# Performance work log

Measured on AMD Instinct MI355X. Metric: run time of the kernel, lower is better.

## Reference

```python
import jax, jax.numpy as jnp
import numpy as np
from jax import lax

NPOINT = 256   # num_proposal
RADIUS = 0.3
NSAMPLE = 16
B, K, C = 32, 1024, 256
OUT_CH = 2 + 3 + 1 * 2 + 18 * 4 + 18  # 97


def _fps(xyz, npoint):
    """Furthest point sampling. xyz (B,N,3) -> indices (B,npoint) int32."""
    b, n, _ = xyz.shape

    def step(carry, _):
        dist, far = carry
        centroid = jnp.take_along_axis(xyz, far[:, None, None], axis=1)  # (B,1,3)
        d = jnp.sum((xyz - centroid) ** 2, -1)
        dist = jnp.minimum(dist, d)
        nxt = jnp.argmax(dist, -1).astype(jnp.int32)
        return (dist, nxt), far

    init = (jnp.full((b, n), 1e10, xyz.dtype), jnp.zeros((b,), jnp.int32))
    _, inds = lax.scan(step, init, None, length=npoint)
    return jnp.transpose(inds)  # (B,npoint)


def _ball_query(new_xyz, xyz, radius, nsample):
    """pointnet2-style ball query: first nsample in-radius neighbors (by point
    order), slots past the count filled with the first found index."""
    n = xyz.shape[1]
    # squared dists (B,P,N) without materializing (B,P,N,3)
    d2 = (jnp.sum(new_xyz ** 2, -1)[:, :, None]
          + jnp.sum(xyz ** 2, -1)[:, None, :]
          - 2.0 * jnp.einsum('bpc,bnc->bpn', new_xyz, xyz))
    key = jnp.where(d2 < radius * radius, jnp.arange(n)[None, None, :], n)
    order = jnp.argsort(key, axis=-1)[:, :, :nsample]
    skey = jnp.take_along_axis(key, order, axis=-1)
    first = order[:, :, :1]
    return jnp.where(skey < n, order, first)  # (B,P,ns)


def _gather_nbrs(pts, idx):
    """pts (B,N,Cd), idx (B,P,ns) -> (B,P,ns,Cd)."""
    b, p, s = idx.shape
    flat = idx.reshape(b, p * s)
    g = jnp.take_along_axis(pts, flat[:, :, None], axis=1)
    return g.reshape(b, p, s, pts.shape[-1])


def setup_inputs() -> dict:
    key = jax.random.key(0)
    ks = jax.random.split(key, 24)
    f32 = jnp.float32

    def w(k, o, c):
        return (jax.random.normal(k, (o, c), f32) / np.float32(np.sqrt(c)))

    def affine(k, o):
        k1, k2 = jax.random.split(k)
        s = 1.0 + 0.1 * jax.random.normal(k1, (o,), f32)
        t = 0.1 * jax.random.normal(k2, (o,), f32)
        return s, t

    d = {}
    d['xyz'] = jax.random.normal(ks[0], (B, K, 3), f32)
    d['features'] = jax.random.normal(ks[1], (B, C, K), f32)
    # SA shared-MLP (conv2d 1x1 + folded eval-mode BN): [C+3 -> 128 -> 128 -> 128]
    d['sa_w0'] = w(ks[2], 128, C + 3); d['sa_s0'], d['sa_t0'] = affine(ks[3], 128)
    d['sa_w1'] = w(ks[4], 128, 128);   d['sa_s1'], d['sa_t1'] = affine(ks[5], 128)
    d['sa_w2'] = w(ks[6], 128, 128);   d['sa_s2'], d['sa_t2'] = affine(ks[7], 128)
    # head conv1d stack: conv1/bn1, conv2/bn2 (BN folded), conv3 with bias
    d['w1'] = w(ks[8], 128, 128); d['s1'], d['t1'] = affine(ks[9], 128)
    d['w2'] = w(ks[10], 128, 128); d['s2'], d['t2'] = affine(ks[11], 128)
    d['w3'] = w(ks[12], OUT_CH, 128)
    d['b3'] = 0.1 * jax.random.normal(ks[13], (OUT_CH,), f32)
    return d


def reference(xyz, features, sa_w0, sa_s0, sa_t0, sa_w1, sa_s1, sa_t1,
              sa_w2, sa_s2, sa_t2, w1, s1, t1, w2, s2, t2, w3, b3):
    # --- PointnetSAModuleVotes (vote_fps branch): FPS + ball query + group ---
    inds = _fps(xyz, NPOINT)                                    # (B,P)
    new_xyz = jnp.take_along_axis(xyz, inds[:, :, None], axis=1)  # (B,P,3)
    idx = _ball_query(new_xyz, xyz, RADIUS, NSAMPLE)            # (B,P,ns)
    # use_xyz=True, normalize_xyz=True
    gx = (_gather_nbrs(xyz, idx) - new_xyz[:, :, None, :]) / RADIUS   # (B,P,ns,3)
    gf = _gather_nbrs(jnp.transpose(features, (0, 2, 1)), idx)        # (B,P,ns,C)
    x = jnp.concatenate([gx, gf], axis=-1)                            # (B,P,ns,C+3)
    # shared MLP (1x1 conv + BN + ReLU), then max-pool over neighbors
    for W, s, t in ((sa_w0, sa_s0, sa_t0), (sa_w1, sa_s1, sa_t1), (sa_w2, sa_s2, sa_t2)):
        x = jax.nn.relu(jnp.einsum('oc,bpnc->bpno', W, x) * s + t)
    f = jnp.transpose(jnp.max(x, axis=2), (0, 2, 1))  # (B,128,P)
    # --- proposal head: conv1d/BN/ReLU x2 + conv1d ---
    h = jax.nn.relu(jnp.einsum('oc,bcp->bop', w1, f) * s1[:, None] + t1[:, None])
    h = jax.nn.relu(jnp.einsum('oc,bcp->bop', w2, h) * s2[:, None] + t2[:, None])
    net = jnp.einsum('oc,bcp->bop', w3, h) + b3[:, None]  # (B,97,P)
    return net
```

## Files before the change

### kernel.cpp

```cpp
#include <hip/hip_runtime.h>

#define NB 32
#define NPTS 1024
#define NP 256
#define NS 16
#define NC 256
#define NH 128
#define NOUT 97
#define RP 16
#define NT (NB * NP)

__global__ __launch_bounds__(256) void prep_kernel(
    const float* __restrict__ sa_w0, const float* __restrict__ sa_w1,
    const float* __restrict__ sa_w2, const float* __restrict__ fc_w1,
    const float* __restrict__ fc_w2, const float* __restrict__ fc_w3,
    float* __restrict__ w0l, float* __restrict__ w0x,
    float* __restrict__ wl1, float* __restrict__ wl2,
    float* __restrict__ fl1, float* __restrict__ fl2,
    float* __restrict__ fl3)
{
  int t = blockIdx.x * 256 + threadIdx.x;
  if (t >= 256 * 128) return;
  int c = t >> 7, o = t & 127;
  w0l[(c * 32 + (o & 31)) * 4 + (o >> 5)] = sa_w0[o * 259 + 3 + c];
  if (c < 3) w0x[c * 128 + o] = sa_w0[o * 259 + c];
  if (c < 128) {
    int qi = (c * 64 + (o & 63)) * 2 + (o >> 6);
    wl1[qi] = sa_w1[o * 128 + c];
    wl2[qi] = sa_w2[o * 128 + c];
    fl1[qi] = fc_w1[o * 128 + c];
    fl2[qi] = fc_w2[o * 128 + c];
    fl3[qi] = (o < NOUT) ? fc_w3[o * 128 + c] : 0.0f;
  }
}

template <int CTRL>
__device__ __forceinline__ float dpp_fmax(float v) {
  float o = __int_as_float(
      __builtin_amdgcn_mov_dpp(__float_as_int(v), CTRL, 0xF, 0xF, true));
  return fmaxf(v, o);
}
template <int CTRL>
__device__ __forceinline__ unsigned dpp_umax(unsigned v) {
  unsigned o = (unsigned)__builtin_amdgcn_mov_dpp((int)v, CTRL, 0xF, 0xF, true);
  return v > o ? v : o;
}

__global__ __launch_bounds__(64) void fused_fps_gfeat_kernel(
    const float* __restrict__ xyz, int* __restrict__ inds,
    const float* __restrict__ features, const float* __restrict__ w0l,
    float* __restrict__ G)
{
  __shared__ __align__(16) float smem[NC * RP];
  const int lane = threadIdx.x;

  if (blockIdx.x < NB) {
    const int b = blockIdx.x;
    const float* xb = xyz + b * NPTS * 3;
    float* s_x = smem;
    float* s_y = smem + NPTS;
    float* s_z = smem + 2 * NPTS;
    float px[16], py[16], pz[16], dist[16];
    const float4* src = reinterpret_cast<const float4*>(xb + lane * 48);
#pragma unroll
    for (int q = 0; q < 4; ++q) {
      float4 v0 = src[3 * q], v1 = src[3 * q + 1], v2 = src[3 * q + 2];
      const float xv[4] = {v0.x, v0.w, v1.z, v2.y};
      const float yv[4] = {v0.y, v1.x, v1.w, v2.z};
      const float zv[4] = {v0.z, v1.y, v2.x, v2.w};
#pragma unroll
      for (int t = 0; t < 4; ++t) {
        int j = 4 * q + t;
        px[j] = xv[t]; py[j] = yv[t]; pz[j] = zv[t];
        s_x[lane * 16 + j] = xv[t];
        s_y[lane * 16 + j] = yv[t];
        s_z[lane * 16 + j] = zv[t];
      }
    }
#pragma unroll
    for (int j = 0; j < 16; ++j) dist[j] = 1e10f;
    int far = 0;
    for (int i = 0; i < NP; ++i) {
      if (lane == 0) inds[b * NP + i] = far;
      float cx = s_x[far], cy = s_y[far], cz = s_z[far];
      float bv = -1.0f; int bi = 0;
#pragma unroll
      for (int j = 0; j < 16; ++j) {
#pragma clang fp contract(off)
        float dx = px[j] - cx;
        float dy = py[j] - cy;
        float dz = pz[j] - cz;
        float d = (dx * dx + dy * dy) + dz * dz;
        float nd = fminf(dist[j], d);
        dist[j] = nd;
        if (nd > bv) { bv = nd; bi = lane * 16 + j; }
      }
      float r = bv;
      r = dpp_fmax<0x111>(r);
      r = dpp_fmax<0x112>(r);
      r = dpp_fmax<0x114>(r);
      r = dpp_fmax<0x118>(r);
      r = dpp_fmax<0x142>(r);
      r = dpp_fmax<0x143>(r);
      float gmax = __int_as_float(__builtin_amdgcn_readlane(__float_as_int(r), 63));
      unsigned cand = (bv == gmax) ? ~(unsigned)bi : 0u;
      cand = dpp_umax<0x111>(cand);
      cand = dpp_umax<0x112>(cand);
      cand = dpp_umax<0x114>(cand);
      cand = dpp_umax<0x118>(cand);
      cand = dpp_umax<0x142>(cand);
      cand = dpp_umax<0x143>(cand);
      unsigned cmax = (unsigned)__builtin_amdgcn_readlane((int)cand, 63);
      far = (int)(~cmax);
    }
    return;
  }

  const int blk = blockIdx.x - NB;
  const int b  = blk >> 6;
  const int n0 = (blk & 63) * 16;
  const int og = lane & 31;
  const int jg = lane >> 5;
  const int joff = jg * 8;
  const float* fb = features + b * NC * NPTS;
#pragma unroll
  for (int r = 0; r < 4; ++r) {
    int c = r * 64 + lane;
    const float4* s4 = reinterpret_cast<const float4*>(fb + c * NPTS + n0);
    float4 v0 = s4[0], v1 = s4[1], v2 = s4[2], v3 = s4[3];
    float* row = smem + c * RP;
    reinterpret_cast<float4*>(row)[0] = v0;
    reinterpret_cast<float4*>(row)[1] = v1;
    reinterpret_cast<float4*>(row)[2] = v2;
    reinterpret_cast<float4*>(row)[3] = v3;
  }
  float acc[4][8];
#pragma unroll
  for (int k = 0; k < 4; ++k)
#pragma unroll
    for (int nn = 0; nn < 8; ++nn) acc[k][nn] = 0.0f;
#pragma unroll 2
  for (int c = 0; c < NC; ++c) {
    const float4 wq = *reinterpret_cast<const float4*>(w0l + (c * 32 + og) * 4);
    const float* row = smem + c * RP + joff;
    const float4 xa = reinterpret_cast<const float4*>(row)[0];
    const float4 xb4 = reinterpret_cast<const float4*>(row)[1];
    const float wk[4] = {wq.x, wq.y, wq.z, wq.w};
    const float xr[8] = {xa.x, xa.y, xa.z, xa.w, xb4.x, xb4.y, xb4.z, xb4.w};
#pragma unroll
    for (int k = 0; k < 4; ++k)
#pragma unroll
      for (int nn = 0; nn < 8; ++nn)
        acc[k][nn] = fmaf(wk[k], xr[nn], acc[k][nn]);
  }
#pragma unroll
  for (int k = 0; k < 4; ++k) {
    int o = og + 32 * k;
    float* gp = G + ((size_t)(b * NPTS + n0 + joff)) * NH + o;
#pragma unroll
    for (int nn = 0; nn < 8; ++nn) gp[nn * NH] = acc[k][nn];
  }
}

__global__ __launch_bounds__(256) void ball_kernel(
    const float* __restrict__ xyz, const int* __restrict__ inds,
    int* __restrict__ nbr, float* __restrict__ gx, int* __restrict__ totals)
{
  const int wid  = blockIdx.x * 4 + (threadIdx.x >> 6);
  const int lane = threadIdx.x & 63;
  const int b = wid >> 8;
  const float* xb = xyz + b * NPTS * 3;
  const int ci = inds[wid];
  const float cx = xb[ci * 3 + 0], cy = xb[ci * 3 + 1], cz = xb[ci * 3 + 2];
  float nq;
  {
#pragma clang fp contract(off)
    nq = (cx * cx + cy * cy) + cz * cz;
  }
  const float R2 = 0.09f;
  unsigned mask = 0;
  int cntj = 0, firstn = NPTS;
  for (int j = 0; j < 16; ++j) {
#pragma clang fp contract(off)
    int n = lane * 16 + j;
    float x = xb[n * 3 + 0], y = xb[n * 3 + 1], z = xb[n * 3 + 2];
    float nx = (x * x + y * y) + z * z;
    float dt = (cx * x + cy * y) + cz * z;
    float d2 = (nq + nx) - 2.0f * dt;
    if (d2 < R2) { mask |= 1u << j; ++cntj; if (firstn == NPTS) firstn = n; }
  }
  int inc = cntj;
  for (int off = 1; off < 64; off <<= 1) {
    int v = __shfl_up(inc, off);
    if (lane >= off) inc += v;
  }
  int rank  = inc - cntj;
  int total = __shfl(inc, 63);
  for (int j = 0; j < 16; ++j) {
    if (mask & (1u << j)) {
      if (rank < NS) {
        int n = lane * 16 + j;
        nbr[wid * NS + rank] = n;
        float x = xb[n * 3 + 0], y = xb[n * 3 + 1], z = xb[n * 3 + 2];
        gx[wid * 48 + rank * 3 + 0] = (x - cx) / 0.3f;
        gx[wid * 48 + rank * 3 + 1] = (y - cy) / 0.3f;
        gx[wid * 48 + rank * 3 + 2] = (z - cz) / 0.3f;
      }
      ++rank;
    }
  }
  int fmin = firstn;
  for (int off2 = 32; off2 > 0; off2 >>= 1) {
    int ov = __shfl_xor(fmin, off2);
    fmin = min(fmin, ov);
  }
  if (lane < NS && lane >= total) {
    nbr[wid * NS + lane] = fmin;
    float x = xb[fmin * 3 + 0], y = xb[fmin * 3 + 1], z = xb[fmin * 3 + 2];
    gx[wid * 48 + lane * 3 + 0] = (x - cx) / 0.3f;
    gx[wid * 48 + lane * 3 + 1] = (y - cy) / 0.3f;
    gx[wid * 48 + lane * 3 + 2] = (z - cz) / 0.3f;
  }
  if (lane == 0) totals[wid] = total;
}

__global__ __launch_bounds__(1024) void scan_kernel(
    const int* __restrict__ totals, int* __restrict__ bucket, int* __restrict__ cnt)
{
  __shared__ unsigned long long ssum[16];
  const int t = threadIdx.x;
  int cls[8];
  unsigned long long local = 0;
#pragma unroll
  for (int k = 0; k < 8; ++k) {
    int tot = totals[t * 8 + k];
    int jc = (tot <= 4) ? 0 : ((tot <= 8) ? 1 : 2);
    cls[k] = jc;
    local += 1ull << (jc * 21);
  }
  unsigned long long inc = local;
  for (int off = 1; off < 64; off <<= 1) {
    unsigned long long v = __shfl_up(inc, off);
    if ((t & 63) >= off) inc += v;
  }
  if ((t & 63) == 63) ssum[t >> 6] = inc;
  __syncthreads();
  if (t == 0) {
    unsigned long long run = 0;
    for (int i = 0; i < 16; ++i) { unsigned long long v = ssum[i]; ssum[i] = run; run += v; }
    cnt[0] = (int)(run & 0x1FFFFFull);
    cnt[1] = (int)((run >> 21) & 0x1FFFFFull);
    cnt[2] = (int)((run >> 42) & 0x1FFFFFull);
  }
  __syncthreads();
  unsigned long long excl = (inc - local) + ssum[t >> 6];
  int p0 = (int)(excl & 0x1FFFFFull);
  int p1 = (int)((excl >> 21) & 0x1FFFFFull);
  int p2 = (int)((excl >> 42) & 0x1FFFFFull);
#pragma unroll
  for (int k = 0; k < 8; ++k) {
    int id = t * 8 + k;
    if (cls[k] == 0)      { bucket[p0] = id; ++p0; }
    else if (cls[k] == 1) { bucket[NT + p1] = id; ++p1; }
    else                  { bucket[2 * NT + p2] = id; ++p2; }
  }
}

__device__ __forceinline__ void mlp16(
    float* __restrict__ xs, const int lane,
    const float* __restrict__ G, const int* __restrict__ idxw,
    const float* __restrict__ gxw,
    const float* __restrict__ w0x, const float* __restrict__ s0v, const float* __restrict__ t0v,
    const float* __restrict__ wl1, const float* __restrict__ s1v, const float* __restrict__ t1v,
    const float* __restrict__ wl2,
    float acc0[16], float acc1[16])
{
  {
    const float wa0 = w0x[lane],      wb0 = w0x[128 + lane],      wc0 = w0x[256 + lane];
    const float wa1 = w0x[64 + lane], wb1 = w0x[192 + lane],      wc1 = w0x[320 + lane];
    const float ss0 = s0v[lane], tt0 = t0v[lane];
    const float ss1 = s0v[64 + lane], tt1 = t0v[64 + lane];
    float r0[16], r1[16];
#pragma unroll
    for (int j = 0; j < 16; ++j) {
      int gj = idxw[j];
      float gxv = gxw[j * 3 + 0], gyv = gxw[j * 3 + 1], gzv = gxw[j * 3 + 2];
      const float* gp = G + (size_t)gj * NH;
      float g0 = gp[lane], g1 = gp[lane + 64];
      float y0 = fmaf(wa0, gxv, fmaf(wb0, gyv, fmaf(wc0, gzv, g0)));
      float y1 = fmaf(wa1, gxv, fmaf(wb1, gyv, fmaf(wc1, gzv, g1)));
      r0[j] = fmaxf(fmaf(y0, ss0, tt0), 0.0f);
      r1[j] = fmaxf(fmaf(y1, ss1, tt1), 0.0f);
    }
#pragma unroll
    for (int q = 0; q < 4; ++q) {
      *reinterpret_cast<float4*>(xs + lane * RP + q * 4) =
          make_float4(r0[4 * q], r0[4 * q + 1], r0[4 * q + 2], r0[4 * q + 3]);
      *reinterpret_cast<float4*>(xs + (lane + 64) * RP + q * 4) =
          make_float4(r1[4 * q], r1[4 * q + 1], r1[4 * q + 2], r1[4 * q + 3]);
    }
  }

#pragma unroll
  for (int j = 0; j < 16; ++j) { acc0[j] = 0.0f; acc1[j] = 0.0f; }
#pragma unroll 2
  for (int c = 0; c < NH; ++c) {
    const float2 wv = *reinterpret_cast<const float2*>(wl1 + (c * 64 + lane) * 2);
#pragma unroll
    for (int q = 0; q < 4; ++q) {
      const float4 xq = *reinterpret_cast<const float4*>(xs + c * RP + q * 4);
      acc0[4 * q + 0] = fmaf(wv.x, xq.x, acc0[4 * q + 0]);
      acc1[4 * q + 0] = fmaf(wv.y, xq.x, acc1[4 * q + 0]);
      acc0[4 * q + 1] = fmaf(wv.x, xq.y, acc0[4 * q + 1]);
      acc1[4 * q + 1] = fmaf(wv.y, xq.y, acc1[4 * q + 1]);
      acc0[4 * q + 2] = fmaf(wv.x, xq.z, acc0[4 * q + 2]);
      acc1[4 * q + 2] = fmaf(wv.y, xq.z, acc1[4 * q + 2]);
      acc0[4 * q + 3] = fmaf(wv.x, xq.w, acc0[4 * q + 3]);
      acc1[4 * q + 3] = fmaf(wv.y, xq.w, acc1[4 * q + 3]);
    }
  }
  {
    const float ssa = s1v[lane], tta = t1v[lane];
    const float ssb = s1v[64 + lane], ttb = t1v[64 + lane];
#pragma unroll
    for (int q = 0; q < 4; ++q) {
      float4 ra, rb;
      ra.x = fmaxf(fmaf(acc0[4 * q + 0], ssa, tta), 0.0f);
      ra.y = fmaxf(fmaf(acc0[4 * q + 1], ssa, tta), 0.0f);
      ra.z = fmaxf(fmaf(acc0[4 * q + 2], ssa, tta), 0.0f);
      ra.w = fmaxf(fmaf(acc0[4 * q + 3], ssa, tta), 0.0f);
      rb.x = fmaxf(fmaf(acc1[4 * q + 0], ssb, ttb), 0.0f);
      rb.y = fmaxf(fmaf(acc1[4 * q + 1], ssb, ttb), 0.0f);
      rb.z = fmaxf(fmaf(acc1[4 * q + 2], ssb, ttb), 0.0f);
      rb.w = fmaxf(fmaf(acc1[4 * q + 3], ssb, ttb), 0.0f);
      *reinterpret_cast<float4*>(xs + lane * RP + q * 4) = ra;
      *reinterpret_cast<float4*>(xs + (lane + 64) * RP + q * 4) = rb;
    }
  }

#pragma unroll
  for (int j = 0; j < 16; ++j) { acc0[j] = 0.0f; acc1[j] = 0.0f; }
#pragma unroll 2
  for (int c = 0; c < NH; ++c) {
    const float2 wv = *reinterpret_cast<const float2*>(wl2 + (c * 64 + lane) * 2);
#pragma unroll
    for (int q = 0; q < 4; ++q) {
      const float4 xq = *reinterpret_cast<const float4*>(xs + c * RP + q * 4);
      acc0[4 * q + 0] = fmaf(wv.x, xq.x, acc0[4 * q + 0]);
      acc1[4 * q + 0] = fmaf(wv.y, xq.x, acc1[4 * q + 0]);
      acc0[4 * q + 1] = fmaf(wv.x, xq.y, acc0[4 * q + 1]);
      acc1[4 * q + 1] = fmaf(wv.y, xq.y, acc1[4 * q + 1]);
      acc0[4 * q + 2] = fmaf(wv.x, xq.z, acc0[4 * q + 2]);
      acc1[4 * q + 2] = fmaf(wv.y, xq.z, acc1[4 * q + 2]);
      acc0[4 * q + 3] = fmaf(wv.x, xq.w, acc0[4 * q + 3]);
      acc1[4 * q + 3] = fmaf(wv.y, xq.w, acc1[4 * q + 3]);
    }
  }
}

template <int TPW>
__device__ __forceinline__ void fc_epilogue(
    float* __restrict__ xs, const int lane, const int tiles[4],
    float acc0[16], float acc1[16],
    const float* __restrict__ s2v, const float* __restrict__ t2v,
    const float* __restrict__ fl1, const float* __restrict__ fs1, const float* __restrict__ ft1,
    const float* __restrict__ fl2, const float* __restrict__ fs2, const float* __restrict__ ft2,
    const float* __restrict__ fl3, const float* __restrict__ b3, float* __restrict__ out)
{
  constexpr int SPT = 16 / TPW;
  {
    const float ssa = s2v[lane], tta = t2v[lane];
    const float ssb = s2v[64 + lane], ttb = t2v[64 + lane];
#pragma unroll
    for (int k = 0; k < TPW; ++k) {
      float fo0 = 0.0f, fo1 = 0.0f;
#pragma unroll
      for (int r = 0; r < SPT; ++r) {
        fo0 = fmaxf(fo0, fmaxf(fmaf(acc0[k * SPT + r], ssa, tta), 0.0f));
        fo1 = fmaxf(fo1, fmaxf(fmaf(acc1[k * SPT + r], ssb, ttb), 0.0f));
      }
      xs[k * 128 + lane] = fo0;
      xs[k * 128 + 64 + lane] = fo1;
    }
  }
  constexpr int HB = TPW * 128;

  float h0[TPW], h1[TPW];

#pragma unroll
  for (int k = 0; k < TPW; ++k) { h0[k] = 0.0f; h1[k] = 0.0f; }
#pragma unroll 4
  for (int c4 = 0; c4 < 32; ++c4) {
    float4 fq[TPW];
#pragma unroll
    for (int k = 0; k < TPW; ++k)
      fq[k] = *reinterpret_cast<const float4*>(xs + k * 128 + c4 * 4);
#pragma unroll
    for (int cc = 0; cc < 4; ++cc) {
      const float2 wv = *reinterpret_cast<const float2*>(fl1 + ((c4 * 4 + cc) * 64 + lane) * 2);
#pragma unroll
      for (int k = 0; k < TPW; ++k) {
        float fv = (cc == 0) ? fq[k].x : (cc == 1) ? fq[k].y : (cc == 2) ? fq[k].z : fq[k].w;
        h0[k] = fmaf(wv.x, fv, h0[k]);
        h1[k] = fmaf(wv.y, fv, h1[k]);
      }
    }
  }
#pragma unroll
  for (int k = 0; k < TPW; ++k) {
    xs[HB + k * 128 + lane]      = fmaxf(fmaf(h0[k], fs1[lane],      ft1[lane]),      0.0f);
    xs[HB + k * 128 + 64 + lane] = fmaxf(fmaf(h1[k], fs1[lane + 64], ft1[lane + 64]), 0.0f);
  }

#pragma unroll
  for (int k = 0; k < TPW; ++k) { h0[k] = 0.0f; h1[k] = 0.0f; }
#pragma unroll 4
  for (int c4 = 0; c4 < 32; ++c4) {
    float4 fq[TPW];
#pragma unroll
    for (int k = 0; k < TPW; ++k)
      fq[k] = *reinterpret_cast<const float4*>(xs + HB + k * 128 + c4 * 4);
#pragma unroll
    for (int cc = 0; cc < 4; ++cc) {
      const float2 wv = *reinterpret_cast<const float2*>(fl2 + ((c4 * 4 + cc) * 64 + lane) * 2);
#pragma unroll
      for (int k = 0; k < TPW; ++k) {
        float fv = (cc == 0) ? fq[k].x : (cc == 1) ? fq[k].y : (cc == 2) ? fq[k].z : fq[k].w;
        h0[k] = fmaf(wv.x, fv, h0[k]);
        h1[k] = fmaf(wv.y, fv, h1[k]);
      }
    }
  }
#pragma unroll
  for (int k = 0; k < TPW; ++k) {
    xs[k * 128 + lane]      = fmaxf(fmaf(h0[k], fs2[lane],      ft2[lane]),      0.0f);
    xs[k * 128 + 64 + lane] = fmaxf(fmaf(h1[k], fs2[lane + 64], ft2[lane + 64]), 0.0f);
  }

#pragma unroll
  for (int k = 0; k < TPW; ++k) { h0[k] = 0.0f; h1[k] = 0.0f; }
#pragma unroll 4
  for (int c4 = 0; c4 < 32; ++c4) {
    float4 fq[TPW];
#pragma unroll
    for (int k = 0; k < TPW; ++k)
      fq[k] = *reinterpret_cast<const float4*>(xs + k * 128 + c4 * 4);
#pragma unroll
    for (int cc = 0; cc < 4; ++cc) {
      const float2 wv = *reinterpret_cast<const float2*>(fl3 + ((c4 * 4 + cc) * 64 + lane) * 2);
#pragma unroll
      for (int k = 0; k < TPW; ++k) {
        float fv = (cc == 0) ? fq[k].x : (cc == 1) ? fq[k].y : (cc == 2) ? fq[k].z : fq[k].w;
        h0[k] = fmaf(wv.x, fv, h0[k]);
        h1[k] = fmaf(wv.y, fv, h1[k]);
      }
    }
  }
#pragma unroll
  for (int k = 0; k < TPW; ++k) {
    int tk = tiles[k];
    int b = tk >> 8, p = tk & 255;
    out[(b * NOUT + lane) * NP + p] = h0[k] + b3[lane];
    if (lane < NOUT - 64)
      out[(b * NOUT + lane + 64) * NP + p] = h1[k] + b3[lane + 64];
  }
}

__global__ __launch_bounds__(512) void main_kernel(
    const int* __restrict__ nbr, const float* __restrict__ gx,
    const int* __restrict__ bucket, const int* __restrict__ cnt,
    const float* __restrict__ G,
    const float* __restrict__ w0x, const float* __restrict__ s0v, const float* __restrict__ t0v,
    const float* __restrict__ wl1, const float* __restrict__ s1v, const float* __restrict__ t1v,
    const float* __restrict__ wl2, const float* __restrict__ s2v, const float* __restrict__ t2v,
    const float* __restrict__ fl1, const float* __restrict__ fs1, const float* __restrict__ ft1,
    const float* __restrict__ fl2, const float* __restrict__ fs2, const float* __restrict__ ft2,
    const float* __restrict__ fl3, const float* __restrict__ b3, float* __restrict__ out)
{
  __shared__ __align__(16) float xt[8][NH * RP];
  __shared__ float gxs[8][NS][3];
  __shared__ int   idxs[8][NS];

  const int w    = threadIdx.x >> 6;
  const int lane = threadIdx.x & 63;
  const int g    = blockIdx.x * 8 + w;

  const int c0 = cnt[0], c1 = cnt[1], c2 = cnt[2];
  const int npack4 = (c0 + 3) >> 2;
  const int npack8 = (c1 + 1) >> 1;
  if (g >= npack4 + npack8 + c2) return;

  int tiles[4];
  int tpw;
  if (g < npack4) {
    tpw = 4;
    tiles[0] = bucket[min(4 * g + 0, c0 - 1)];
    tiles[1] = bucket[min(4 * g + 1, c0 - 1)];
    tiles[2] = bucket[min(4 * g + 2, c0 - 1)];
    tiles[3] = bucket[min(4 * g + 3, c0 - 1)];
  } else if (g < npack4 + npack8) {
    tpw = 2;
    int base = g - npack4;
    tiles[0] = bucket[NT + min(2 * base + 0, c1 - 1)];
    tiles[1] = bucket[NT + min(2 * base + 1, c1 - 1)];
    tiles[2] = tiles[0]; tiles[3] = tiles[1];
  } else {
    tpw = 1;
    tiles[0] = bucket[2 * NT + (g - npack4 - npack8)];
    tiles[1] = tiles[2] = tiles[3] = tiles[0];
  }

  float* xs = &xt[w][0];

  if (lane < 16) {
    int tk, r;
    if (tpw == 4)      { tk = (lane < 4) ? tiles[0] : (lane < 8) ? tiles[1]
                              : (lane < 12) ? tiles[2] : tiles[3];  r = lane & 3; }
    else if (tpw == 2) { tk = (lane < 8) ? tiles[0] : tiles[1];     r = lane & 7; }
    else               { tk = tiles[0];                              r = lane; }
    int bk = tk >> 8;
    idxs[w][lane] = bk * NPTS + nbr[tk * NS + r];
    gxs[w][lane][0] = gx[tk * 48 + r * 3 + 0];
    gxs[w][lane][1] = gx[tk * 48 + r * 3 + 1];
    gxs[w][lane][2] = gx[tk * 48 + r * 3 + 2];
  }

  float acc0[16], acc1[16];
  mlp16(xs, lane, G, idxs[w], &gxs[w][0][0],
        w0x, s0v, t0v, wl1, s1v, t1v, wl2, acc0, acc1);

  if (tpw == 4) {
    fc_epilogue<4>(xs, lane, tiles, acc0, acc1, s2v, t2v,
                   fl1, fs1, ft1, fl2, fs2, ft2, fl3, b3, out);
  } else if (tpw == 2) {
    fc_epilogue<2>(xs, lane, tiles, acc0, acc1, s2v, t2v,
                   fl1, fs1, ft1, fl2, fs2, ft2, fl3, b3, out);
  } else {
    fc_epilogue<1>(xs, lane, tiles, acc0, acc1, s2v, t2v,
                   fl1, fs1, ft1, fl2, fs2, ft2, fl3, b3, out);
  }
}

extern "C" void kernel_launch(void* const* d_in, const int* in_sizes, int n_in,
                              void* d_out, int out_size, void* d_ws, size_t ws_size,
                              hipStream_t stream) {
  const float* xyz      = (const float*)d_in[0];
  const float* features = (const float*)d_in[1];
  const float* sa_w0 = (const float*)d_in[2];
  const float* sa_s0 = (const float*)d_in[3];
  const float* sa_t0 = (const float*)d_in[4];
  const float* sa_w1 = (const float*)d_in[5];
  const float* sa_s1 = (const float*)d_in[6];
  const float* sa_t1 = (const float*)d_in[7];
  const float* sa_w2 = (const float*)d_in[8];
  const float* sa_s2 = (const float*)d_in[9];
  const float* sa_t2 = (const float*)d_in[10];
  const float* fc_w1 = (const float*)d_in[11];
  const float* fc_s1 = (const float*)d_in[12];
  const float* fc_t1 = (const float*)d_in[13];
  const float* fc_w2 = (const float*)d_in[14];
  const float* fc_s2 = (const float*)d_in[15];
  const float* fc_t2 = (const float*)d_in[16];
  const float* fc_w3 = (const float*)d_in[17];
  const float* fc_b3 = (const float*)d_in[18];
  float* out = (float*)d_out;

  char* ws = (char*)d_ws;
  int* inds = (int*)ws;            ws += (size_t)NT * sizeof(int);
  float* w0l  = (float*)ws;        ws += (size_t)256 * 128 * sizeof(float);
  float* w0x  = (float*)ws;        ws += (size_t)3 * 128 * sizeof(float);
  float* wl1  = (float*)ws;        ws += (size_t)128 * 128 * sizeof(float);
  float* wl2  = (float*)ws;        ws += (size_t)128 * 128 * sizeof(float);
  float* fl1  = (float*)ws;        ws += (size_t)128 * 128 * sizeof(float);
  float* fl2  = (float*)ws;        ws += (size_t)128 * 128 * sizeof(float);
  float* fl3  = (float*)ws;        ws += (size_t)128 * 128 * sizeof(float);
  float* G    = (float*)ws;        ws += (size_t)NB * NPTS * NH * sizeof(float);
  int*   nbr  = (int*)ws;          ws += (size_t)NT * NS * sizeof(int);
  float* gx   = (float*)ws;        ws += (size_t)NT * 48 * sizeof(float);
  int* totals = (int*)ws;          ws += (size_t)NT * sizeof(int);
  int* bucket = (int*)ws;          ws += (size_t)3 * NT * sizeof(int);
  int* cnt    = (int*)ws;          ws += 16 * sizeof(int);

  prep_kernel<<<128, 256, 0, stream>>>(sa_w0, sa_w1, sa_w2, fc_w1, fc_w2, fc_w3,
                                       w0l, w0x, wl1, wl2, fl1, fl2, fl3);
  fused_fps_gfeat_kernel<<<NB + NB * (NPTS / 16), 64, 0, stream>>>(
      xyz, inds, features, w0l, G);
  ball_kernel<<<NT / 4, 256, 0, stream>>>(xyz, inds, nbr, gx, totals);
  scan_kernel<<<1, 1024, 0, stream>>>(totals, bucket, cnt);
  main_kernel<<<NT / 8, 512, 0, stream>>>(
      nbr, gx, bucket, cnt, G,
      w0x, sa_s0, sa_t0,
      wl1, sa_s1, sa_t1,
      wl2, sa_s2, sa_t2,
      fl1, fc_s1, fc_t1,
      fl2, fc_s2, fc_t2,
      fl3, fc_b3, out);
}
```

Baseline: 251.9 us.

## Split FPS into own kernel, fuse feature GEMM with ball query, tree argmax

FPS moves into a standalone kernel. The first-layer feature projection (G) is no longer fused with FPS; it now shares a launch with the ball query, which runs as one 64-thread block per centroid. The per-lane argmax inside FPS becomes a pairwise tree reduction instead of a sequential compare chain, which shortens the dependency chain on the serial FPS critical path. The cost is that the G projection can no longer overlap FPS: it now waits until FPS finishes, which may lengthen the critical path.

```diff
diff --git a/kernel.cpp b/kernel.cpp
--- a/kernel.cpp
+++ b/kernel.cpp
@@ -9,6 +9,7 @@
 #define NOUT 97
 #define RP 16
 #define NT (NB * NP)
+#define NGF (NB * (NPTS / 16))
 
 __global__ __launch_bounds__(256) void prep_kernel(
     const float* __restrict__ sa_w0, const float* __restrict__ sa_w1,
@@ -46,128 +47,145 @@
   return v > o ? v : o;
 }
 
-__global__ __launch_bounds__(64) void fused_fps_gfeat_kernel(
-    const float* __restrict__ xyz, int* __restrict__ inds,
+__global__ __launch_bounds__(64) void fps_kernel(const float* __restrict__ xyz,
+                                                 int* __restrict__ inds)
+{
+  __shared__ __align__(16) float smem[NPTS * 3];
+  const int lane = threadIdx.x;
+  const int b = blockIdx.x;
+  const float* xb = xyz + b * NPTS * 3;
+  float* s_x = smem;
+  float* s_y = smem + NPTS;
+  float* s_z = smem + 2 * NPTS;
+  float px[16], py[16], pz[16], dist[16];
+  const float4* src = reinterpret_cast<const float4*>(xb + lane * 48);
+#pragma unroll
+  for (int q = 0; q < 4; ++q) {
+    float4 v0 = src[3 * q], v1 = src[3 * q + 1], v2 = src[3 * q + 2];
+    const float xv[4] = {v0.x, v0.w, v1.z, v2.y};
+    const float yv[4] = {v0.y, v1.x, v1.w, v2.z};
+    const float zv[4] = {v0.z, v1.y, v2.x, v2.w};
+#pragma unroll
+    for (int t = 0; t < 4; ++t) {
+      int j = 4 * q + t;
+      px[j] = xv[t]; py[j] = yv[t]; pz[j] = zv[t];
+      s_x[lane * 16 + j] = xv[t];
+      s_y[lane * 16 + j] = yv[t];
+      s_z[lane * 16 + j] = zv[t];
+    }
+  }
+#pragma unroll
+  for (int j = 0; j < 16; ++j) dist[j] = 1e10f;
+  int far = 0;
+  for (int i = 0; i < NP; ++i) {
+    if (lane == 0) inds[b * NP + i] = far;
+    float cx = s_x[far], cy = s_y[far], cz = s_z[far];
+#pragma unroll
+    for (int j = 0; j < 16; ++j) {
+#pragma clang fp contract(off)
+      float dx = px[j] - cx;
+      float dy = py[j] - cy;
+      float dz = pz[j] - cz;
+      float d = (dx * dx + dy * dy) + dz * dz;
+      dist[j] = fminf(dist[j], d);
+    }
+    float v8[8]; int i8[8];
+#pragma unroll
+    for (int t = 0; t < 8; ++t) {
+      bool r = dist[2 * t + 1] > dist[2 * t];
+      v8[t] = r ? dist[2 * t + 1] : dist[2 * t];
+      i8[t] = r ? 2 * t + 1 : 2 * t;
+    }
+    float v4[4]; int i4[4];
+#pragma unroll
+    for (int t = 0; t < 4; ++t) {
+      bool r = v8[2 * t + 1] > v8[2 * t];
+      v4[t] = r ? v8[2 * t + 1] : v8[2 * t];
+      i4[t] = r ? i8[2 * t + 1] : i8[2 * t];
+    }
+    float v2a, v2b; int i2a, i2b;
+    { bool r = v4[1] > v4[0]; v2a = r ? v4[1] : v4[0]; i2a = r ? i4[1] : i4[0]; }
+    { bool r = v4[3] > v4[2]; v2b = r ? v4[3] : v4[2]; i2b = r ? i4[3] : i4[2]; }
+    float bv; int bi;
+    { bool r = v2b > v2a; bv = r ? v2b : v2a; bi = lane * 16 + (r ? i2b : i2a); }
+    float r = bv;
+    r = dpp_fmax<0x111>(r);
+    r = dpp_fmax<0x112>(r);
+    r = dpp_fmax<0x114>(r);
+    r = dpp_fmax<0x118>(r);
+    r = dpp_fmax<0x142>(r);
+    r = dpp_fmax<0x143>(r);
+    float gmax = __int_as_float(__builtin_amdgcn_readlane(__float_as_int(r), 63));
+    unsigned cand = (bv == gmax) ? ~(unsigned)bi : 0u;
+    cand = dpp_umax<0x111>(cand);
+    cand = dpp_umax<0x112>(cand);
+    cand = dpp_umax<0x114>(cand);
+    cand = dpp_umax<0x118>(cand);
+    cand = dpp_umax<0x142>(cand);
+    cand = dpp_umax<0x143>(cand);
+    unsigned cmax = (unsigned)__builtin_amdgcn_readlane((int)cand, 63);
+    far = (int)(~cmax);
+  }
+}
+
+__global__ __launch_bounds__(64) void gfeat_ball_kernel(
+    const float* __restrict__ xyz, const int* __restrict__ inds,
     const float* __restrict__ features, const float* __restrict__ w0l,
-    float* __restrict__ G)
+    float* __restrict__ G,
+    int* __restrict__ nbr, float* __restrict__ gx, int* __restrict__ totals)
 {
   __shared__ __align__(16) float smem[NC * RP];
   const int lane = threadIdx.x;
 
-  if (blockIdx.x < NB) {
-    const int b = blockIdx.x;
-    const float* xb = xyz + b * NPTS * 3;
-    float* s_x = smem;
-    float* s_y = smem + NPTS;
-    float* s_z = smem + 2 * NPTS;
-    float px[16], py[16], pz[16], dist[16];
-    const float4* src = reinterpret_cast<const float4*>(xb + lane * 48);
-#pragma unroll
-    for (int q = 0; q < 4; ++q) {
-      float4 v0 = src[3 * q], v1 = src[3 * q + 1], v2 = src[3 * q + 2];
-      const float xv[4] = {v0.x, v0.w, v1.z, v2.y};
-      const float yv[4] = {v0.y, v1.x, v1.w, v2.z};
-      const float zv[4] = {v0.z, v1.y, v2.x, v2.w};
-#pragma unroll
-      for (int t = 0; t < 4; ++t) {
-        int j = 4 * q + t;
-        px[j] = xv[t]; py[j] = yv[t]; pz[j] = zv[t];
-        s_x[lane * 16 + j] = xv[t];
-        s_y[lane * 16 + j] = yv[t];
-        s_z[lane * 16 + j] = zv[t];
-      }
-    }
-#pragma unroll
-    for (int j = 0; j < 16; ++j) dist[j] = 1e10f;
-    int far = 0;
-    for (int i = 0; i < NP; ++i) {
-      if (lane == 0) inds[b * NP + i] = far;
-      float cx = s_x[far], cy = s_y[far], cz = s_z[far];
-      float bv = -1.0f; int bi = 0;
-#pragma unroll
-      for (int j = 0; j < 16; ++j) {
-#pragma clang fp contract(off)
-        float dx = px[j] - cx;
-        float dy = py[j] - cy;
-        float dz = pz[j] - cz;
-        float d = (dx * dx + dy * dy) + dz * dz;
-        float nd = fminf(dist[j], d);
-        dist[j] = nd;
-        if (nd > bv) { bv = nd; bi = lane * 16 + j; }
-      }
-      float r = bv;
-      r = dpp_fmax<0x111>(r);
-      r = dpp_fmax<0x112>(r);
-      r = dpp_fmax<0x114>(r);
-      r = dpp_fmax<0x118>(r);
-      r = dpp_fmax<0x142>(r);
-      r = dpp_fmax<0x143>(r);
-      float gmax = __int_as_float(__builtin_amdgcn_readlane(__float_as_int(r), 63));
-      unsigned cand = (bv == gmax) ? ~(unsigned)bi : 0u;
-      cand = dpp_umax<0x111>(cand);
-      cand = dpp_umax<0x112>(cand);
-      cand = dpp_umax<0x114>(cand);
-      cand = dpp_umax<0x118>(cand);
-      cand = dpp_umax<0x142>(cand);
-      cand = dpp_umax<0x143>(cand);
-      unsigned cmax = (unsigned)__builtin_amdgcn_readlane((int)cand, 63);
-      far = (int)(~cmax);
+  if (blockIdx.x < NGF) {
+    const int blk = blockIdx.x;
+    const int b  = blk >> 6;
+    const int n0 = (blk & 63) * 16;
+    const int og = lane & 31;
+    const int jg = lane >> 5;
+    const int joff = jg * 8;
+    const float* fb = features + b * NC * NPTS;
+#pragma unroll
+    for (int r = 0; r < 4; ++r) {
+      int c = r * 64 + lane;
+      const float4* s4 = reinterpret_cast<const float4*>(fb + c * NPTS + n0);
+      float4 v0 = s4[0], v1 = s4[1], v2 = s4[2], v3 = s4[3];
+      float* row = smem + c * RP;
+      reinterpret_cast<float4*>(row)[0] = v0;
+      reinterpret_cast<float4*>(row)[1] = v1;
+      reinterpret_cast<float4*>(row)[2] = v2;
+      reinterpret_cast<float4*>(row)[3] = v3;
+    }
+    float acc[4][8];
+#pragma unroll
+    for (int k = 0; k < 4; ++k)
+#pragma unroll
+      for (int nn = 0; nn < 8; ++nn) acc[k][nn] = 0.0f;
+#pragma unroll 2
+    for (int c = 0; c < NC; ++c) {
+      const float4 wq = *reinterpret_cast<const float4*>(w0l + (c * 32 + og) * 4);
+      const float* row = smem + c * RP + joff;
+      const float4 xa = reinterpret_cast<const float4*>(row)[0];
+      const float4 xb4 = reinterpret_cast<const float4*>(row)[1];
+      const float wk[4] = {wq.x, wq.y, wq.z, wq.w};
+      const float xr[8] = {xa.x, xa.y, xa.z, xa.w, xb4.x, xb4.y, xb4.z, xb4.w};
+#pragma unroll
+      for (int k = 0; k < 4; ++k)
+#pragma unroll
+        for (int nn = 0; nn < 8; ++nn)
+          acc[k][nn] = fmaf(wk[k], xr[nn], acc[k][nn]);
+    }
+#pragma unroll
+    for (int k = 0; k < 4; ++k) {
+      int o = og + 32 * k;
+      float* gp = G + ((size_t)(b * NPTS + n0 + joff)) * NH + o;
+#pragma unroll
+      for (int nn = 0; nn < 8; ++nn) gp[nn * NH] = acc[k][nn];
     }
     return;
   }
 
-  const int blk = blockIdx.x - NB;
-  const int b  = blk >> 6;
-  const int n0 = (blk & 63) * 16;
-  const int og = lane & 31;
-  const int jg = lane >> 5;
-  const int joff = jg * 8;
-  const float* fb = features + b * NC * NPTS;
-#pragma unroll
-  for (int r = 0; r < 4; ++r) {
-    int c = r * 64 + lane;
-    const float4* s4 = reinterpret_cast<const float4*>(fb + c * NPTS + n0);
-    float4 v0 = s4[0], v1 = s4[1], v2 = s4[2], v3 = s4[3];
-    float* row = smem + c * RP;
-    reinterpret_cast<float4*>(row)[0] = v0;
-    reinterpret_cast<float4*>(row)[1] = v1;
-    reinterpret_cast<float4*>(row)[2] = v2;
-    reinterpret_cast<float4*>(row)[3] = v3;
-  }
-  float acc[4][8];
-#pragma unroll
-  for (int k = 0; k < 4; ++k)
-#pragma unroll
-    for (int nn = 0; nn < 8; ++nn) acc[k][nn] = 0.0f;
-#pragma unroll 2
-  for (int c = 0; c < NC; ++c) {
-    const float4 wq = *reinterpret_cast<const float4*>(w0l + (c * 32 + og) * 4);
-    const float* row = smem + c * RP + joff;
-    const float4 xa = reinterpret_cast<const float4*>(row)[0];
-    const float4 xb4 = reinterpret_cast<const float4*>(row)[1];
-    const float wk[4] = {wq.x, wq.y, wq.z, wq.w};
-    const float xr[8] = {xa.x, xa.y, xa.z, xa.w, xb4.x, xb4.y, xb4.z, xb4.w};
-#pragma unroll
-    for (int k = 0; k < 4; ++k)
-#pragma unroll
-      for (int nn = 0; nn < 8; ++nn)
-        acc[k][nn] = fmaf(wk[k], xr[nn], acc[k][nn]);
-  }
-#pragma unroll
-  for (int k = 0; k < 4; ++k) {
-    int o = og + 32 * k;
-    float* gp = G + ((size_t)(b * NPTS + n0 + joff)) * NH + o;
-#pragma unroll
-    for (int nn = 0; nn < 8; ++nn) gp[nn * NH] = acc[k][nn];
-  }
-}
-
-__global__ __launch_bounds__(256) void ball_kernel(
-    const float* __restrict__ xyz, const int* __restrict__ inds,
-    int* __restrict__ nbr, float* __restrict__ gx, int* __restrict__ totals)
-{
-  const int wid  = blockIdx.x * 4 + (threadIdx.x >> 6);
-  const int lane = threadIdx.x & 63;
+  const int wid = blockIdx.x - NGF;
   const int b = wid >> 8;
   const float* xb = xyz + b * NPTS * 3;
   const int ci = inds[wid];
@@ -583,9 +601,9 @@
 
   prep_kernel<<<128, 256, 0, stream>>>(sa_w0, sa_w1, sa_w2, fc_w1, fc_w2, fc_w3,
                                        w0l, w0x, wl1, wl2, fl1, fl2, fl3);
-  fused_fps_gfeat_kernel<<<NB + NB * (NPTS / 16), 64, 0, stream>>>(
-      xyz, inds, features, w0l, G);
-  ball_kernel<<<NT / 4, 256, 0, stream>>>(xyz, inds, nbr, gx, totals);
+  fps_kernel<<<NB, 64, 0, stream>>>(xyz, inds);
+  gfeat_ball_kernel<<<NGF + NT, 64, 0, stream>>>(
+      xyz, inds, features, w0l, G, nbr, gx, totals);
   scan_kernel<<<1, 1024, 0, stream>>>(totals, bucket, cnt);
   main_kernel<<<NT / 8, 512, 0, stream>>>(
       nbr, gx, bucket, cnt, G,
```

Result: slower. 337.8 us (+34.1%).

## Interleave two batches per FPS wavefront and fuse the argmax reduction

Applied to the files above, without the earlier changes.

Each furthest-point-sampling wavefront now handles two batches at once, interleaving their distance updates and cross-lane reductions. This gives the serial, latency-bound 256-step loop independent work to hide DPP and LDS latency. The separate max and index reductions are merged into one pass over a (value bits, inverted index) key, which keeps first-index tie-breaking. In exchange, register pressure per wave rises and shared memory grows to 24KB for every block, including the feature-GEMM blocks, which may lower their occupancy.

```diff
diff --git a/kernel.cpp b/kernel.cpp
--- a/kernel.cpp
+++ b/kernel.cpp
@@ -9,6 +9,7 @@
 #define NOUT 97
 #define RP 16
 #define NT (NB * NP)
+#define NGF (NB * (NPTS / 16))
 
 __global__ __launch_bounds__(256) void prep_kernel(
     const float* __restrict__ sa_w0, const float* __restrict__ sa_w1,
@@ -34,89 +35,98 @@
   }
 }
 
-template <int CTRL>
-__device__ __forceinline__ float dpp_fmax(float v) {
-  float o = __int_as_float(
-      __builtin_amdgcn_mov_dpp(__float_as_int(v), CTRL, 0xF, 0xF, true));
-  return fmaxf(v, o);
-}
-template <int CTRL>
-__device__ __forceinline__ unsigned dpp_umax(unsigned v) {
-  unsigned o = (unsigned)__builtin_amdgcn_mov_dpp((int)v, CTRL, 0xF, 0xF, true);
-  return v > o ? v : o;
-}
-
-__global__ __launch_bounds__(64) void fused_fps_gfeat_kernel(
+#define KSTEP(CTRL) \
+  { unsigned ohiA = (unsigned)__builtin_amdgcn_mov_dpp((int)hiA, CTRL, 0xF, 0xF, true); \
+    unsigned oloA = (unsigned)__builtin_amdgcn_mov_dpp((int)loA, CTRL, 0xF, 0xF, true); \
+    unsigned ohiB = (unsigned)__builtin_amdgcn_mov_dpp((int)hiB, CTRL, 0xF, 0xF, true); \
+    unsigned oloB = (unsigned)__builtin_amdgcn_mov_dpp((int)loB, CTRL, 0xF, 0xF, true); \
+    bool gA = (ohiA > hiA) || (ohiA == hiA && oloA > loA); \
+    hiA = gA ? ohiA : hiA; loA = gA ? oloA : loA; \
+    bool gB = (ohiB > hiB) || (ohiB == hiB && oloB > loB); \
+    hiB = gB ? ohiB : hiB; loB = gB ? oloB : loB; }
+
+__global__ __launch_bounds__(64) void fps2_gfeat_kernel(
     const float* __restrict__ xyz, int* __restrict__ inds,
     const float* __restrict__ features, const float* __restrict__ w0l,
     float* __restrict__ G)
 {
-  __shared__ __align__(16) float smem[NC * RP];
+  __shared__ __align__(16) float smem[NPTS * 6];
   const int lane = threadIdx.x;
 
-  if (blockIdx.x < NB) {
-    const int b = blockIdx.x;
-    const float* xb = xyz + b * NPTS * 3;
-    float* s_x = smem;
-    float* s_y = smem + NPTS;
-    float* s_z = smem + 2 * NPTS;
-    float px[16], py[16], pz[16], dist[16];
-    const float4* src = reinterpret_cast<const float4*>(xb + lane * 48);
+  if (blockIdx.x < NB / 2) {
+    const int b0 = blockIdx.x * 2;
+    const float* xbA = xyz + (size_t)b0 * NPTS * 3;
+    const float* xbB = xbA + NPTS * 3;
+    float* sAx = smem;            float* sAy = smem + NPTS;     float* sAz = smem + 2 * NPTS;
+    float* sBx = smem + 3 * NPTS; float* sBy = smem + 4 * NPTS; float* sBz = smem + 5 * NPTS;
+    float pxA[16], pyA[16], pzA[16], dA[16];
+    float pxB[16], pyB[16], pzB[16], dB[16];
+    const float4* srcA = reinterpret_cast<const float4*>(xbA + lane * 48);
+    const float4* srcB = reinterpret_cast<const float4*>(xbB + lane * 48);
 #pragma unroll
     for (int q = 0; q < 4; ++q) {
-      float4 v0 = src[3 * q], v1 = src[3 * q + 1], v2 = src[3 * q + 2];
-      const float xv[4] = {v0.x, v0.w, v1.z, v2.y};
-      const float yv[4] = {v0.y, v1.x, v1.w, v2.z};
-      const float zv[4] = {v0.z, v1.y, v2.x, v2.w};
+      float4 a0 = srcA[3 * q], a1 = srcA[3 * q + 1], a2 = srcA[3 * q + 2];
+      float4 b0v = srcB[3 * q], b1v = srcB[3 * q + 1], b2v = srcB[3 * q + 2];
+      const float axv[4] = {a0.x, a0.w, a1.z, a2.y};
+      const float ayv[4] = {a0.y, a1.x, a1.w, a2.z};
+      const float azv[4] = {a0.z, a1.y, a2.x, a2.w};
+      const float bxv[4] = {b0v.x, b0v.w, b1v.z, b2v.y};
+      const float byv[4] = {b0v.y, b1v.x, b1v.w, b2v.z};
+      const float bzv[4] = {b0v.z, b1v.y, b2v.x, b2v.w};
 #pragma unroll
       for (int t = 0; t < 4; ++t) {
         int j = 4 * q + t;
-        px[j] = xv[t]; py[j] = yv[t]; pz[j] = zv[t];
-        s_x[lane * 16 + j] = xv[t];
-        s_y[lane * 16 + j] = yv[t];
-        s_z[lane * 16 + j] = zv[t];
-      }
-    }
-#pragma unroll
-    for (int j = 0; j < 16; ++j) dist[j] = 1e10f;
-    int far = 0;
+        pxA[j] = axv[t]; pyA[j] = ayv[t]; pzA[j] = azv[t];
+        pxB[j] = bxv[t]; pyB[j] = byv[t]; pzB[j] = bzv[t];
+        sAx[lane * 16 + j] = axv[t];
+        sAy[lane * 16 + j] = ayv[t];
+        sAz[lane * 16 + j] = azv[t];
+        sBx[lane * 16 + j] = bxv[t];
+        sBy[lane * 16 + j] = byv[t];
+        sBz[lane * 16 + j] = bzv[t];
+      }
+    }
+#pragma unroll
+    for (int j = 0; j < 16; ++j) { dA[j] = 1e10f; dB[j] = 1e10f; }
+    int farA = 0, farB = 0;
     for (int i = 0; i < NP; ++i) {
-      if (lane == 0) inds[b * NP + i] = far;
-      float cx = s_x[far], cy = s_y[far], cz = s_z[far];
-      float bv = -1.0f; int bi = 0;
+      if (lane == 0) {
+        inds[b0 * NP + i] = farA;
+        inds[(b0 + 1) * NP + i] = farB;
+      }
+      float cxA = sAx[farA], cyA = sAy[farA], czA = sAz[farA];
+      float cxB = sBx[farB], cyB = sBy[farB], czB = sBz[farB];
+      float bvA = -1.0f; int biA = 0;
+      float bvB = -1.0f; int biB = 0;
 #pragma unroll
       for (int j = 0; j < 16; ++j) {
 #pragma clang fp contract(off)
-        float dx = px[j] - cx;
-        float dy = py[j] - cy;
-        float dz = pz[j] - cz;
-        float d = (dx * dx + dy * dy) + dz * dz;
-        float nd = fminf(dist[j], d);
-        dist[j] = nd;
-        if (nd > bv) { bv = nd; bi = lane * 16 + j; }
-      }
-      float r = bv;
-      r = dpp_fmax<0x111>(r);
-      r = dpp_fmax<0x112>(r);
-      r = dpp_fmax<0x114>(r);
-      r = dpp_fmax<0x118>(r);
-      r = dpp_fmax<0x142>(r);
-      r = dpp_fmax<0x143>(r);
-      float gmax = __int_as_float(__builtin_amdgcn_readlane(__float_as_int(r), 63));
-      unsigned cand = (bv == gmax) ? ~(unsigned)bi : 0u;
-      cand = dpp_umax<0x111>(cand);
-      cand = dpp_umax<0x112>(cand);
-      cand = dpp_umax<0x114>(cand);
-      cand = dpp_umax<0x118>(cand);
-      cand = dpp_umax<0x142>(cand);
-      cand = dpp_umax<0x143>(cand);
-      unsigned cmax = (unsigned)__builtin_amdgcn_readlane((int)cand, 63);
-      far = (int)(~cmax);
+        float dxA = pxA[j] - cxA, dyA = pyA[j] - cyA, dzA = pzA[j] - czA;
+        float ddA = (dxA * dxA + dyA * dyA) + dzA * dzA;
+        float ndA = fminf(dA[j], ddA);
+        dA[j] = ndA;
+        if (ndA > bvA) { bvA = ndA; biA = lane * 16 + j; }
+        float dxB = pxB[j] - cxB, dyB = pyB[j] - cyB, dzB = pzB[j] - czB;
+        float ddB = (dxB * dxB + dyB * dyB) + dzB * dzB;
+        float ndB = fminf(dB[j], ddB);
+        dB[j] = ndB;
+        if (ndB > bvB) { bvB = ndB; biB = lane * 16 + j; }
+      }
+      unsigned hiA = __float_as_uint(bvA), loA = 1023u - (unsigned)biA;
+      unsigned hiB = __float_as_uint(bvB), loB = 1023u - (unsigned)biB;
+      KSTEP(0x111)
+      KSTEP(0x112)
+      KSTEP(0x114)
+      KSTEP(0x118)
+      KSTEP(0x142)
+      KSTEP(0x143)
+      farA = 1023 - (int)(unsigned)__builtin_amdgcn_readlane((int)loA, 63);
+      farB = 1023 - (int)(unsigned)__builtin_amdgcn_readlane((int)loB, 63);
     }
     return;
   }
 
-  const int blk = blockIdx.x - NB;
+  const int blk = blockIdx.x - NB / 2;
   const int b  = blk >> 6;
   const int n0 = (blk & 63) * 16;
   const int og = lane & 31;
@@ -583,7 +593,7 @@
 
   prep_kernel<<<128, 256, 0, stream>>>(sa_w0, sa_w1, sa_w2, fc_w1, fc_w2, fc_w3,
                                        w0l, w0x, wl1, wl2, fl1, fl2, fl3);
-  fused_fps_gfeat_kernel<<<NB + NB * (NPTS / 16), 64, 0, stream>>>(
+  fps2_gfeat_kernel<<<NB / 2 + NGF, 64, 0, stream>>>(
       xyz, inds, features, w0l, G);
   ball_kernel<<<NT / 4, 256, 0, stream>>>(xyz, inds, nbr, gx, totals);
   scan_kernel<<<1, 1024, 0, stream>>>(totals, bucket, cnt);
```

New measurement: 380.5 us. 1.51x slower.
